# Optimization experiments

Hardware: AMD Instinct MI355X
Metric: run time of the kernel (lower is better)

Reference implementation:

```python
import jax, jax.numpy as jnp
import numpy as np

B, C, H, W = 8, 256, 48, 48

def setup_inputs() -> dict:
    key = jax.random.key(0)
    ks = jax.random.split(key, 8)
    s = 1.0 / np.sqrt(C)  # conv2d default init scale (uniform fan_in)
    x = jax.random.normal(ks[0], (B, C, H, W), dtype=jnp.float32)
    y = jax.random.normal(ks[1], (B, C, H, W), dtype=jnp.float32)
    Wq = jax.random.uniform(ks[2], (C, C), jnp.float32, -s, s)
    bq = jax.random.uniform(ks[3], (C,), jnp.float32, -s, s)
    Wk = jax.random.uniform(ks[4], (C, C), jnp.float32, -s, s)
    bk = jax.random.uniform(ks[5], (C,), jnp.float32, -s, s)
    Wv = jax.random.uniform(ks[6], (C, C), jnp.float32, -s, s)
    bv = jax.random.uniform(ks[7], (C,), jnp.float32, -s, s)
    return {"x": x, "y": y, "Wq": Wq, "bq": bq, "Wk": Wk, "bk": bk, "Wv": Wv, "bv": bv}

def reference(x, y, Wq, bq, Wk, bk, Wv, bv):
    b, c, h, w = x.shape
    n = h * w
    # [B,C,H,W] -> tokens [B,N,C]
    xt = x.reshape(b, c, n).transpose(0, 2, 1)
    yt = y.reshape(b, c, n).transpose(0, 2, 1)
    # 1x1 convs == per-token linear projections
    q = xt @ Wq.T + bq  # [B,N,C]
    k = yt @ Wk.T + bk  # [B,N,C]
    v = yt @ Wv.T + bv  # [B,N,C]
    # unscaled QK^T softmax (module applies no 1/sqrt(d) scaling)
    scores = jnp.einsum('bnc,bmc->bnm', q, k)  # [B,N,N]
    attn = jax.nn.softmax(scores, axis=-1)
    out = jnp.einsum('bnm,bmc->bnc', attn, v)  # [B,N,C]
    return out.transpose(0, 2, 1).reshape(b, c, h, w)
```

## Files before the change

kernel.cpp:

```cpp
#include <hip/hip_runtime.h>
#include <stdint.h>

#define Bb 8
#define Cc 256
#define Nn 2304
#define PQT 36
#define QT 18
#define KSPLIT 3
#define TPS 24
#define L2E 1.44269504088896f
#define DEFER_THR 8.0f

#define AS1 __attribute__((address_space(1)))
#define AS3 __attribute__((address_space(3)))

typedef unsigned short u16;
typedef unsigned int u32;
typedef _Float16 h16;
typedef h16  h16x8 __attribute__((ext_vector_type(8)));
typedef u16  u16x8 __attribute__((ext_vector_type(8)));
typedef u16  u16x4 __attribute__((ext_vector_type(4)));
typedef u32  u32x4 __attribute__((ext_vector_type(4)));
typedef float f32x4 __attribute__((ext_vector_type(4)));
typedef float f32x2 __attribute__((ext_vector_type(2)));

static __device__ __forceinline__ u16 f2h(float f) {
  return __builtin_bit_cast(u16, (h16)f);
}
static __device__ __forceinline__ float h2f(u16 v) {
  return (float)__builtin_bit_cast(h16, v);
}
static __device__ __forceinline__ h16x8 ash(u16x8 v) {
  return __builtin_bit_cast(h16x8, v);
}
static __device__ __forceinline__ f32x4 mfma16(u16x8 a, u16x8 b, f32x4 c) {
  return __builtin_amdgcn_mfma_f32_16x16x32_f16(ash(a), ash(b), c, 0, 0, 0);
}
static __device__ __forceinline__ u32 pkf16(float a, float b) {
  return __builtin_bit_cast(u32, __builtin_amdgcn_cvt_pkrtz(a, b));
}

__global__ __launch_bounds__(256, 3) void proj_kernel(
    const float* __restrict__ x, const float* __restrict__ y,
    const float* __restrict__ Wq, const float* __restrict__ Wk,
    const float* __restrict__ Wv,
    const float* __restrict__ bq, const float* __restrict__ bk,
    const float* __restrict__ bv,
    u16* __restrict__ Qf, u16* __restrict__ Kf, u16* __restrict__ Vf)
{
  __shared__ u16 sW[32 * 256];
  const int t    = threadIdx.x;
  const int b    = blockIdx.x;
  const int q0   = blockIdx.y * 64;
  const int z    = blockIdx.z;
  const int lane = t & 63;
  const int w    = t >> 6;
  const int quad = lane >> 4;
  const int l15  = lane & 15;

  const float* src = (z == 0) ? x : y;
  const int tok = q0 + w * 16 + l15;
  u16x8 af[8];
#pragma unroll
  for (int kc = 0; kc < 8; ++kc) {
    const float* p = src + ((size_t)b * Cc + kc * 32 + quad * 8) * Nn + tok;
    float v[8];
#pragma unroll
    for (int j = 0; j < 8; ++j) v[j] = p[(size_t)j * Nn];
#pragma unroll
    for (int j = 0; j < 8; ++j) af[kc][j] = f2h(v[j]);
  }

  const int npass = z + 1;
#pragma unroll 1
  for (int pass = 0; pass < npass; ++pass) {
    const float* W32 = (z == 0) ? Wq : (pass == 0 ? Wk : Wv);
    const bool vpass = (z == 1) && (pass == 1);

    f32x4 acc[16];
#pragma unroll
    for (int i = 0; i < 16; ++i) acc[i] = (f32x4){0.f, 0.f, 0.f, 0.f};

#pragma unroll 1
    for (int rg = 0; rg < 8; ++rg) {
      __syncthreads();
#pragma unroll
      for (int it = 0; it < 4; ++it) {
        const int id = it * 256 + t;
        const int row = id >> 5, gch = id & 31;
        const float* wp = W32 + (size_t)(rg * 32 + row) * 256 + gch * 8;
        const f32x4 a = *(const f32x4*)wp;
        const f32x4 c2 = *(const f32x4*)(wp + 4);
        u16x8 ov;
#pragma unroll
        for (int j = 0; j < 4; ++j) { ov[j] = f2h(a[j]); ov[j + 4] = f2h(c2[j]); }
        *(u16x8*)(sW + row * 256 + ((gch ^ (row & 7)) << 3)) = ov;
      }
      __syncthreads();
      if (!vpass) {
#pragma unroll
        for (int cbl = 0; cbl < 2; ++cbl) {
          const int rl = cbl * 16 + l15;
          f32x4 a = acc[rg * 2 + cbl];
#pragma unroll
          for (int kc = 0; kc < 8; ++kc) {
            const u16x8 bf = *(const u16x8*)(sW + rl * 256 + (((kc * 4 + quad) ^ (rl & 7)) << 3));
            a = mfma16(af[kc], bf, a);
          }
          acc[rg * 2 + cbl] = a;
        }
      } else {
#pragma unroll
        for (int mt = 0; mt < 2; ++mt) {
          const int rl = mt * 16 + l15;
          f32x4 a = acc[rg * 2 + mt];
#pragma unroll
          for (int kc = 0; kc < 8; ++kc) {
            const u16x8 wfr = *(const u16x8*)(sW + rl * 256 + (((kc * 4 + quad) ^ (rl & 7)) << 3));
            a = mfma16(wfr, af[kc], a);
          }
          acc[rg * 2 + mt] = a;
        }
      }
    }

    if (!vpass) {
      const float* bias = (z == 0) ? bq : bk;
      u16* O = (z == 0) ? Qf : Kf;
#pragma unroll
      for (int cb = 0; cb < 16; ++cb) {
        const int co = cb * 16 + l15;
        const float bs = bias[co];
        const size_t base = ((size_t)b * Nn + q0 + w * 16 + quad * 4) * Cc + co;
#pragma unroll
        for (int r = 0; r < 4; ++r)
          O[base + (size_t)r * Cc] = f2h(acc[cb][r] + bs);
      }
    } else {
#pragma unroll
      for (int cb = 0; cb < 16; ++cb) {
        const int crow = cb * 16 + quad * 4;
#pragma unroll
        for (int r = 0; r < 4; ++r)
          Vf[((size_t)b * Cc + crow + r) * Nn + q0 + w * 16 + l15] =
              f2h(acc[cb][r] + bv[crow + r]);
      }
    }
  }
}

__global__ __launch_bounds__(256, 2) void attn_kernel(
    const u16* __restrict__ Qf, const u16* __restrict__ Kf,
    const u16* __restrict__ Vf, u16* __restrict__ OpH,
    float* __restrict__ Ml)
{
  __shared__ u16 sK[32 * 256];
  __shared__ u16 sV[256 * 32];
  const int t    = threadIdx.x;
  const int b    = blockIdx.x;
  const int q0   = blockIdx.y * 128;
  const int sp   = blockIdx.z;
  const int lane = t & 63;
  const int w    = t >> 6;
  const int quad = lane >> 4;
  const int l15  = lane & 15;
  const int wq0  = q0 + w * 32;

  u16x8 qf[2][8];
#pragma unroll
  for (int g = 0; g < 2; ++g) {
    const size_t qrow = ((size_t)b * Nn + wq0 + g * 16 + l15) * Cc;
#pragma unroll
    for (int kc = 0; kc < 8; ++kc)
      qf[g][kc] = *(const u16x8*)(Qf + qrow + kc * 32 + quad * 8);
  }

  f32x4 o[2][16];
#pragma unroll
  for (int g = 0; g < 2; ++g)
#pragma unroll
    for (int i = 0; i < 16; ++i) o[g][i] = (f32x4){0.f, 0.f, 0.f, 0.f};
  float mrow[2] = {-3e38f, -3e38f};
  float lrow[2] = {0.f, 0.f};

  const u16* Kb = Kf + (size_t)b * Nn * Cc;
  const u16* Vb = Vf + (size_t)b * Cc * Nn;

  const int rbase = 2 * w + (lane >> 5);
  const int kcol  = ((lane & 31) ^ rbase) << 3;
  const int rb2 = rbase >> 2, rb3 = rbase & 3;
  int koff[4];
#pragma unroll
  for (int it = 0; it < 4; ++it) {
    const int key = (((rb2 + 2 * it) & 3) << 3) + rb3 + ((it >> 1) << 2);
    koff[it] = key * Cc + kcol;
  }
  const u16* Kt = Kb + (size_t)(sp * TPS * 32) * Cc;
  const int cV   = w * 16 + (lane >> 2);
  const int vcol = ((lane & 3) ^ ((cV >> 1) & 3)) << 3;
  const u16* vp0 = Vb + (size_t)cV * Nn + sp * TPS * 32 + vcol;

  auto stage = [&](int kb) {
#pragma unroll
    for (int it = 0; it < 4; ++it) {
      __builtin_amdgcn_global_load_lds(
          (const AS1 void*)(Kt + (size_t)kb * 32 * Cc + koff[it]),
          (AS3 void*)&sK[(w + 4 * it) * 512], 16, 0, 0);
      __builtin_amdgcn_global_load_lds(
          (const AS1 void*)(vp0 + kb * 32 + (size_t)it * 64 * Nn),
          (AS3 void*)&sV[(w + 4 * it) * 512], 16, 0, 0);
    }
  };

  stage(0);

  const int vbase = l15 * 32 + ((quad ^ ((l15 >> 1) & 3)) << 3);

#pragma unroll 1
  for (int kb = 0; kb < TPS; ++kb) {
    __builtin_amdgcn_s_waitcnt(0x0F70);
    __syncthreads();

    f32x4 s[2][2];
    s[0][0] = (f32x4){0.f, 0.f, 0.f, 0.f}; s[0][1] = s[0][0];
    s[1][0] = s[0][0];                      s[1][1] = s[0][0];
#pragma unroll
    for (int kc = 0; kc < 8; ++kc) {
      const int ch = ((kc * 4 + quad) ^ (l15 & 7)) << 3;
      const u16x8 k0 = *(const u16x8*)(sK + l15 * 256 + ch);
      const u16x8 k1 = *(const u16x8*)(sK + (16 + l15) * 256 + ch);
      s[0][0] = mfma16(k0, qf[0][kc], s[0][0]);
      s[0][1] = mfma16(k1, qf[0][kc], s[0][1]);
      s[1][0] = mfma16(k0, qf[1][kc], s[1][0]);
      s[1][1] = mfma16(k1, qf[1][kc], s[1][1]);
    }

    u16x8 pf[2];
    float al[2];
    int needany = 0;
#pragma unroll
    for (int g = 0; g < 2; ++g) {
      float mloc = fmaxf(
          fmaxf(fmaxf(s[g][0][0], s[g][0][1]), fmaxf(s[g][0][2], s[g][0][3])),
          fmaxf(fmaxf(s[g][1][0], s[g][1][1]), fmaxf(s[g][1][2], s[g][1][3])));
      mloc = fmaxf(mloc, __shfl_xor(mloc, 16, 64));
      mloc = fmaxf(mloc, __shfl_xor(mloc, 32, 64));
      const bool need = mloc > mrow[g] + DEFER_THR;
      const float mn  = need ? mloc : mrow[g];
      al[g] = need ? exp2f((mrow[g] - mn) * L2E) : 1.f;
      mrow[g] = mn;
      needany |= (int)need;

      float p[8];
      float sum = 0.f;
#pragma unroll
      for (int r = 0; r < 4; ++r) {
        p[r]     = exp2f((s[g][0][r] - mn) * L2E);
        p[4 + r] = exp2f((s[g][1][r] - mn) * L2E);
        sum += p[r] + p[4 + r];
      }
      sum += __shfl_xor(sum, 16, 64);
      sum += __shfl_xor(sum, 32, 64);
      lrow[g] = lrow[g] * al[g] + sum;

      u32x4 pw;
      pw[0] = pkf16(p[0], p[1]);
      pw[1] = pkf16(p[2], p[3]);
      pw[2] = pkf16(p[4], p[5]);
      pw[3] = pkf16(p[6], p[7]);
      pf[g] = __builtin_bit_cast(u16x8, pw);
    }

    if (__any(needany)) {
#pragma unroll
      for (int i = 0; i < 16; ++i) {
#pragma unroll
        for (int r = 0; r < 4; ++r) {
          o[0][i][r] *= al[0];
          o[1][i][r] *= al[1];
        }
      }
    }

#pragma unroll
    for (int cb = 0; cb < 16; ++cb) {
      const u16x8 vf = *(const u16x8*)(sV + cb * 512 + vbase);
      o[0][cb] = mfma16(vf, pf[0], o[0][cb]);
      o[1][cb] = mfma16(vf, pf[1], o[1][cb]);
    }

    __syncthreads();
    if (kb + 1 < TPS) stage(kb + 1);
  }

  u16* Ob = OpH + ((size_t)sp * Bb + b) * (size_t)Cc * Nn;
#pragma unroll
  for (int g = 0; g < 2; ++g) {
    const float inv = 1.f / lrow[g];
    const int qn = wq0 + g * 16 + l15;
#pragma unroll
    for (int cb = 0; cb < 16; ++cb) {
#pragma unroll
      for (int r = 0; r < 4; ++r)
        Ob[(size_t)(cb * 16 + quad * 4 + r) * Nn + qn] = f2h(o[g][cb][r] * inv);
    }
  }
  if (lane < 16) {
    float* mlb = Ml + ((size_t)sp * Bb + b) * (size_t)Nn * 2;
#pragma unroll
    for (int g = 0; g < 2; ++g) {
      const int qn = wq0 + g * 16 + l15;
      *(f32x2*)(mlb + (size_t)qn * 2) = (f32x2){mrow[g], lrow[g]};
    }
  }
}

__global__ void merge_kernel(const u16* __restrict__ OpH,
                             const float* __restrict__ Ml,
                             float* __restrict__ out)
{
  const int idx = blockIdx.x * 256 + threadIdx.x;
  const int n4 = idx % 576;
  const int bc = idx / 576;
  const int b  = bc >> 8;
  const size_t obase = (size_t)bc * Nn + n4 * 4;

  float oh[KSPLIT][4], mv[KSPLIT][4], lv[KSPLIT][4];
#pragma unroll
  for (int s = 0; s < KSPLIT; ++s) {
    const u16x4 hv = *(const u16x4*)(OpH + ((size_t)s * Bb * Cc + bc) * Nn + n4 * 4);
#pragma unroll
    for (int j = 0; j < 4; ++j) oh[s][j] = h2f(hv[j]);
    const float* ml = Ml + ((size_t)s * Bb + b) * (size_t)Nn * 2 + n4 * 8;
    const f32x4 u0 = *(const f32x4*)ml;
    const f32x4 u1 = *(const f32x4*)(ml + 4);
#pragma unroll
    for (int j = 0; j < 4; ++j) {
      mv[s][j] = (j < 2) ? u0[j * 2]     : u1[(j - 2) * 2];
      lv[s][j] = (j < 2) ? u0[j * 2 + 1] : u1[(j - 2) * 2 + 1];
    }
  }

  f32x4 r;
#pragma unroll
  for (int j = 0; j < 4; ++j) {
    float m = mv[0][j];
#pragma unroll
    for (int s = 1; s < KSPLIT; ++s) m = fmaxf(m, mv[s][j]);
    float num = 0.f, den = 0.f;
#pragma unroll
    for (int s = 0; s < KSPLIT; ++s) {
      const float ws = lv[s][j] * exp2f((mv[s][j] - m) * L2E);
      num += oh[s][j] * ws;
      den += ws;
    }
    r[j] = num / den;
  }
  *(f32x4*)(out + obase) = r;
}

extern "C" void kernel_launch(void* const* d_in, const int* in_sizes, int n_in,
                              void* d_out, int out_size, void* d_ws, size_t ws_size,
                              hipStream_t stream) {
  const float* x  = (const float*)d_in[0];
  const float* y  = (const float*)d_in[1];
  const float* Wq = (const float*)d_in[2];
  const float* bq = (const float*)d_in[3];
  const float* Wk = (const float*)d_in[4];
  const float* bk = (const float*)d_in[5];
  const float* Wv = (const float*)d_in[6];
  const float* bv = (const float*)d_in[7];
  float* out = (float*)d_out;

  const size_t NC = (size_t)Bb * Nn * Cc;
  u16* Qf = (u16*)d_ws;
  u16* Kf = Qf + NC;
  u16* Vf = Kf + NC;
  u16* OpH = Vf + NC;
  float* Ml = (float*)(OpH + (size_t)KSPLIT * NC);

  hipLaunchKernelGGL(proj_kernel, dim3(Bb, PQT, 2), dim3(256), 0, stream,
                     x, y, Wq, Wk, Wv, bq, bk, bv, Qf, Kf, Vf);
  hipLaunchKernelGGL(attn_kernel, dim3(Bb, QT, KSPLIT), dim3(256), 0, stream,
                     Qf, Kf, Vf, OpH, Ml);
  hipLaunchKernelGGL(merge_kernel, dim3(4608), dim3(256), 0, stream,
                     OpH, Ml, out);
}
```

Before: 262.9 us.

## Pre-convert weights to fp16 and double-buffer LDS staging in projection and attention

Measured after the change: 227.9 us. 13.3% less time.

```diff
diff --git a/kernel.cpp b/kernel.cpp
--- a/kernel.cpp
+++ b/kernel.cpp
@@ -4,7 +4,7 @@
 #define Bb 8
 #define Cc 256
 #define Nn 2304
-#define PQT 36
+#define PJT 18
 #define QT 18
 #define KSPLIT 3
 #define TPS 24
@@ -40,110 +40,131 @@
   return __builtin_bit_cast(u32, __builtin_amdgcn_cvt_pkrtz(a, b));
 }
 
-__global__ __launch_bounds__(256, 3) void proj_kernel(
+__global__ void prep_kernel(const float* __restrict__ Wq,
+                            const float* __restrict__ Wk,
+                            const float* __restrict__ Wv,
+                            u16* __restrict__ Wf)
+{
+  const int tid = blockIdx.x * 256 + threadIdx.x;
+  const int m   = tid >> 13;
+  const int off = (tid & 8191) * 8;
+  const float* src = (m == 0) ? Wq : (m == 1) ? Wk : Wv;
+  const f32x4 a = *(const f32x4*)(src + off);
+  const f32x4 c = *(const f32x4*)(src + off + 4);
+  u16x8 o;
+#pragma unroll
+  for (int j = 0; j < 4; ++j) { o[j] = f2h(a[j]); o[j + 4] = f2h(c[j]); }
+  *(u16x8*)(Wf + (size_t)m * 65536 + off) = o;
+}
+
+__global__ __launch_bounds__(256, 2) void proj_kernel(
     const float* __restrict__ x, const float* __restrict__ y,
-    const float* __restrict__ Wq, const float* __restrict__ Wk,
-    const float* __restrict__ Wv,
+    const u16* __restrict__ Wf,
     const float* __restrict__ bq, const float* __restrict__ bk,
     const float* __restrict__ bv,
     u16* __restrict__ Qf, u16* __restrict__ Kf, u16* __restrict__ Vf)
 {
-  __shared__ u16 sW[32 * 256];
+  __shared__ u16 sW[2][32 * 256];
   const int t    = threadIdx.x;
   const int b    = blockIdx.x;
-  const int q0   = blockIdx.y * 64;
+  const int q0   = blockIdx.y * 128;
   const int z    = blockIdx.z;
   const int lane = t & 63;
   const int w    = t >> 6;
   const int quad = lane >> 4;
   const int l15  = lane & 15;
 
+  const u16* WZ = Wf + (size_t)z * 65536;
+
+  const int rbase = 2 * w + (lane >> 5);
+  const int wcol  = ((lane & 31) ^ rbase) << 3;
+
+  auto stage = [&](int rg, int buf) {
+#pragma unroll
+    for (int it = 0; it < 4; ++it) {
+      __builtin_amdgcn_global_load_lds(
+          (const AS1 void*)(WZ + (size_t)(rg * 32 + rbase + 8 * it) * 256 + wcol),
+          (AS3 void*)&sW[buf][(w + 4 * it) * 512], 16, 0, 0);
+    }
+  };
+
+  stage(0, 0);
+
   const float* src = (z == 0) ? x : y;
-  const int tok = q0 + w * 16 + l15;
-  u16x8 af[8];
-#pragma unroll
-  for (int kc = 0; kc < 8; ++kc) {
-    const float* p = src + ((size_t)b * Cc + kc * 32 + quad * 8) * Nn + tok;
-    float v[8];
-#pragma unroll
-    for (int j = 0; j < 8; ++j) v[j] = p[(size_t)j * Nn];
-#pragma unroll
-    for (int j = 0; j < 8; ++j) af[kc][j] = f2h(v[j]);
-  }
-
-  const int npass = z + 1;
+  u16x8 af[2][8];
+#pragma unroll
+  for (int g = 0; g < 2; ++g) {
+    const int tok = q0 + g * 64 + w * 16 + l15;
+#pragma unroll
+    for (int kc = 0; kc < 8; ++kc) {
+      const float* p = src + ((size_t)b * Cc + kc * 32 + quad * 8) * Nn + tok;
+      float v[8];
+#pragma unroll
+      for (int j = 0; j < 8; ++j) v[j] = p[(size_t)j * Nn];
+#pragma unroll
+      for (int j = 0; j < 8; ++j) af[g][kc][j] = f2h(v[j]);
+    }
+  }
+
+  f32x4 acc[2][16];
+#pragma unroll
+  for (int g = 0; g < 2; ++g)
+#pragma unroll
+    for (int i = 0; i < 16; ++i) acc[g][i] = (f32x4){0.f, 0.f, 0.f, 0.f};
+
+  int cur = 0;
 #pragma unroll 1
-  for (int pass = 0; pass < npass; ++pass) {
-    const float* W32 = (z == 0) ? Wq : (pass == 0 ? Wk : Wv);
-    const bool vpass = (z == 1) && (pass == 1);
-
-    f32x4 acc[16];
-#pragma unroll
-    for (int i = 0; i < 16; ++i) acc[i] = (f32x4){0.f, 0.f, 0.f, 0.f};
-
-#pragma unroll 1
-    for (int rg = 0; rg < 8; ++rg) {
-      __syncthreads();
-#pragma unroll
-      for (int it = 0; it < 4; ++it) {
-        const int id = it * 256 + t;
-        const int row = id >> 5, gch = id & 31;
-        const float* wp = W32 + (size_t)(rg * 32 + row) * 256 + gch * 8;
-        const f32x4 a = *(const f32x4*)wp;
-        const f32x4 c2 = *(const f32x4*)(wp + 4);
-        u16x8 ov;
-#pragma unroll
-        for (int j = 0; j < 4; ++j) { ov[j] = f2h(a[j]); ov[j + 4] = f2h(c2[j]); }
-        *(u16x8*)(sW + row * 256 + ((gch ^ (row & 7)) << 3)) = ov;
-      }
-      __syncthreads();
-      if (!vpass) {
-#pragma unroll
-        for (int cbl = 0; cbl < 2; ++cbl) {
-          const int rl = cbl * 16 + l15;
-          f32x4 a = acc[rg * 2 + cbl];
-#pragma unroll
-          for (int kc = 0; kc < 8; ++kc) {
-            const u16x8 bf = *(const u16x8*)(sW + rl * 256 + (((kc * 4 + quad) ^ (rl & 7)) << 3));
-            a = mfma16(af[kc], bf, a);
-          }
-          acc[rg * 2 + cbl] = a;
-        }
-      } else {
-#pragma unroll
-        for (int mt = 0; mt < 2; ++mt) {
-          const int rl = mt * 16 + l15;
-          f32x4 a = acc[rg * 2 + mt];
-#pragma unroll
-          for (int kc = 0; kc < 8; ++kc) {
-            const u16x8 wfr = *(const u16x8*)(sW + rl * 256 + (((kc * 4 + quad) ^ (rl & 7)) << 3));
-            a = mfma16(wfr, af[kc], a);
-          }
-          acc[rg * 2 + mt] = a;
+  for (int rg = 0; rg < 8; ++rg) {
+    __builtin_amdgcn_s_waitcnt(0x0F70);
+    __syncthreads();
+    if (rg + 1 < 8) stage(rg + 1, cur ^ 1);
+#pragma unroll
+    for (int cbl = 0; cbl < 2; ++cbl) {
+      const int rl = cbl * 16 + l15;
+      f32x4 a0 = acc[0][rg * 2 + cbl];
+      f32x4 a1 = acc[1][rg * 2 + cbl];
+#pragma unroll
+      for (int kc = 0; kc < 8; ++kc) {
+        const u16x8 bf = *(const u16x8*)(sW[cur] + rl * 256 + (((kc * 4 + quad) ^ (rl & 7)) << 3));
+        if (z < 2) {
+          a0 = mfma16(af[0][kc], bf, a0);
+          a1 = mfma16(af[1][kc], bf, a1);
+        } else {
+          a0 = mfma16(bf, af[0][kc], a0);
+          a1 = mfma16(bf, af[1][kc], a1);
         }
       }
-    }
-
-    if (!vpass) {
-      const float* bias = (z == 0) ? bq : bk;
-      u16* O = (z == 0) ? Qf : Kf;
+      acc[0][rg * 2 + cbl] = a0;
+      acc[1][rg * 2 + cbl] = a1;
+    }
+    cur ^= 1;
+  }
+
+  if (z < 2) {
+    const float* bias = (z == 0) ? bq : bk;
+    u16* O = (z == 0) ? Qf : Kf;
+#pragma unroll
+    for (int g = 0; g < 2; ++g) {
 #pragma unroll
       for (int cb = 0; cb < 16; ++cb) {
         const int co = cb * 16 + l15;
         const float bs = bias[co];
-        const size_t base = ((size_t)b * Nn + q0 + w * 16 + quad * 4) * Cc + co;
+        const size_t base = ((size_t)b * Nn + q0 + g * 64 + w * 16 + quad * 4) * Cc + co;
 #pragma unroll
         for (int r = 0; r < 4; ++r)
-          O[base + (size_t)r * Cc] = f2h(acc[cb][r] + bs);
+          O[base + (size_t)r * Cc] = f2h(acc[g][cb][r] + bs);
       }
-    } else {
+    }
+  } else {
+#pragma unroll
+    for (int g = 0; g < 2; ++g) {
 #pragma unroll
       for (int cb = 0; cb < 16; ++cb) {
         const int crow = cb * 16 + quad * 4;
 #pragma unroll
         for (int r = 0; r < 4; ++r)
-          Vf[((size_t)b * Cc + crow + r) * Nn + q0 + w * 16 + l15] =
-              f2h(acc[cb][r] + bv[crow + r]);
+          Vf[((size_t)b * Cc + crow + r) * Nn + q0 + g * 64 + w * 16 + l15] =
+              f2h(acc[g][cb][r] + bv[crow + r]);
       }
     }
   }
@@ -154,8 +175,8 @@
     const u16* __restrict__ Vf, u16* __restrict__ OpH,
     float* __restrict__ Ml)
 {
-  __shared__ u16 sK[32 * 256];
-  __shared__ u16 sV[256 * 32];
+  __shared__ u16 sK[2][32 * 256];
+  __shared__ u16 sV[2][256 * 32];
   const int t    = threadIdx.x;
   const int b    = blockIdx.x;
   const int q0   = blockIdx.y * 128;
@@ -166,23 +187,6 @@
   const int l15  = lane & 15;
   const int wq0  = q0 + w * 32;
 
-  u16x8 qf[2][8];
-#pragma unroll
-  for (int g = 0; g < 2; ++g) {
-    const size_t qrow = ((size_t)b * Nn + wq0 + g * 16 + l15) * Cc;
-#pragma unroll
-    for (int kc = 0; kc < 8; ++kc)
-      qf[g][kc] = *(const u16x8*)(Qf + qrow + kc * 32 + quad * 8);
-  }
-
-  f32x4 o[2][16];
-#pragma unroll
-  for (int g = 0; g < 2; ++g)
-#pragma unroll
-    for (int i = 0; i < 16; ++i) o[g][i] = (f32x4){0.f, 0.f, 0.f, 0.f};
-  float mrow[2] = {-3e38f, -3e38f};
-  float lrow[2] = {0.f, 0.f};
-
   const u16* Kb = Kf + (size_t)b * Nn * Cc;
   const u16* Vb = Vf + (size_t)b * Cc * Nn;
 
@@ -200,26 +204,45 @@
   const int vcol = ((lane & 3) ^ ((cV >> 1) & 3)) << 3;
   const u16* vp0 = Vb + (size_t)cV * Nn + sp * TPS * 32 + vcol;
 
-  auto stage = [&](int kb) {
+  auto stage = [&](int kb, int buf) {
 #pragma unroll
     for (int it = 0; it < 4; ++it) {
       __builtin_amdgcn_global_load_lds(
           (const AS1 void*)(Kt + (size_t)kb * 32 * Cc + koff[it]),
-          (AS3 void*)&sK[(w + 4 * it) * 512], 16, 0, 0);
+          (AS3 void*)&sK[buf][(w + 4 * it) * 512], 16, 0, 0);
       __builtin_amdgcn_global_load_lds(
           (const AS1 void*)(vp0 + kb * 32 + (size_t)it * 64 * Nn),
-          (AS3 void*)&sV[(w + 4 * it) * 512], 16, 0, 0);
+          (AS3 void*)&sV[buf][(w + 4 * it) * 512], 16, 0, 0);
     }
   };
 
-  stage(0);
+  stage(0, 0);
+
+  u16x8 qf[2][8];
+#pragma unroll
+  for (int g = 0; g < 2; ++g) {
+    const size_t qrow = ((size_t)b * Nn + wq0 + g * 16 + l15) * Cc;
+#pragma unroll
+    for (int kc = 0; kc < 8; ++kc)
+      qf[g][kc] = *(const u16x8*)(Qf + qrow + kc * 32 + quad * 8);
+  }
+
+  f32x4 o[2][16];
+#pragma unroll
+  for (int g = 0; g < 2; ++g)
+#pragma unroll
+    for (int i = 0; i < 16; ++i) o[g][i] = (f32x4){0.f, 0.f, 0.f, 0.f};
+  float mrow[2] = {-3e38f, -3e38f};
+  float lrow[2] = {0.f, 0.f};
 
   const int vbase = l15 * 32 + ((quad ^ ((l15 >> 1) & 3)) << 3);
 
+  int cur = 0;
 #pragma unroll 1
   for (int kb = 0; kb < TPS; ++kb) {
     __builtin_amdgcn_s_waitcnt(0x0F70);
     __syncthreads();
+    if (kb + 1 < TPS) stage(kb + 1, cur ^ 1);
 
     f32x4 s[2][2];
     s[0][0] = (f32x4){0.f, 0.f, 0.f, 0.f}; s[0][1] = s[0][0];
@@ -227,8 +250,8 @@
 #pragma unroll
     for (int kc = 0; kc < 8; ++kc) {
       const int ch = ((kc * 4 + quad) ^ (l15 & 7)) << 3;
-      const u16x8 k0 = *(const u16x8*)(sK + l15 * 256 + ch);
-      const u16x8 k1 = *(const u16x8*)(sK + (16 + l15) * 256 + ch);
+      const u16x8 k0 = *(const u16x8*)(sK[cur] + l15 * 256 + ch);
+      const u16x8 k1 = *(const u16x8*)(sK[cur] + (16 + l15) * 256 + ch);
       s[0][0] = mfma16(k0, qf[0][kc], s[0][0]);
       s[0][1] = mfma16(k1, qf[0][kc], s[0][1]);
       s[1][0] = mfma16(k0, qf[1][kc], s[1][0]);
@@ -284,13 +307,12 @@
 
 #pragma unroll
     for (int cb = 0; cb < 16; ++cb) {
-      const u16x8 vf = *(const u16x8*)(sV + cb * 512 + vbase);
+      const u16x8 vf = *(const u16x8*)(sV[cur] + cb * 512 + vbase);
       o[0][cb] = mfma16(vf, pf[0], o[0][cb]);
       o[1][cb] = mfma16(vf, pf[1], o[1][cb]);
     }
 
-    __syncthreads();
-    if (kb + 1 < TPS) stage(kb + 1);
+    cur ^= 1;
   }
 
   u16* Ob = OpH + ((size_t)sp * Bb + b) * (size_t)Cc * Nn;
@@ -376,11 +398,14 @@
   u16* Qf = (u16*)d_ws;
   u16* Kf = Qf + NC;
   u16* Vf = Kf + NC;
-  u16* OpH = Vf + NC;
+  u16* Wf = Vf + NC;
+  u16* OpH = Wf + 3 * 65536;
   float* Ml = (float*)(OpH + (size_t)KSPLIT * NC);
 
-  hipLaunchKernelGGL(proj_kernel, dim3(Bb, PQT, 2), dim3(256), 0, stream,
-                     x, y, Wq, Wk, Wv, bq, bk, bv, Qf, Kf, Vf);
+  hipLaunchKernelGGL(prep_kernel, dim3(96), dim3(256), 0, stream,
+                     Wq, Wk, Wv, Wf);
+  hipLaunchKernelGGL(proj_kernel, dim3(Bb, PJT, 3), dim3(256), 0, stream,
+                     x, y, Wf, bq, bk, bv, Qf, Kf, Vf);
   hipLaunchKernelGGL(attn_kernel, dim3(Bb, QT, KSPLIT), dim3(256), 0, stream,
                      Qf, Kf, Vf, OpH, Ml);
   hipLaunchKernelGGL(merge_kernel, dim3(4608), dim3(256), 0, stream,
```
